# Performance work log

Measured on AMD Instinct MI355X. Metric: run time of the kernel, lower is better.

Reference implementation:

```python
import jax, jax.numpy as jnp
import numpy as np

N = 100000
E = 1600000
GENE = 512
HID = 128
NCLS = 10
EPS = 1e-5  # BatchNorm1d default eps


def setup_inputs() -> dict:
    key = jax.random.key(0)
    ks = jax.random.split(key, 16)
    def lin(k, fan_in, fan_out):
        return (jax.random.normal(k, (fan_in, fan_out), jnp.float32) / np.sqrt(fan_in)).astype(jnp.float32)
    dims = [(GENE, HID), (HID, 2 * HID), (2 * HID, HID), (HID, HID // 2)]
    inp = {}
    inp["x"] = jax.random.normal(ks[0], (N, GENE), jnp.float32)
    inp["edge_index"] = jax.random.randint(ks[1], (2, E), 0, N)
    for i, (di, do) in enumerate(dims, start=1):
        inp[f"W{i}"] = lin(ks[1 + i], di, do)
        inp[f"b{i}"] = jnp.zeros((do,), jnp.float32)
        inp[f"g{i}"] = jnp.ones((do,), jnp.float32)     # BN gamma
        inp[f"beta{i}"] = jnp.zeros((do,), jnp.float32)  # BN beta
    inp["Wc"] = lin(ks[10], HID // 2, NCLS)
    inp["bc"] = jnp.zeros((NCLS,), jnp.float32)
    return inp


def gcn_conv(h_in, W, b, src, dst, deg_inv_sqrt):
    # PyG GCNConv: transform, then symmetric-normalized aggregation with self-loops
    h = h_in @ W                                   # [N, out]
    norm = (deg_inv_sqrt[src] * deg_inv_sqrt[dst])[:, None]  # [E, 1]
    agg = jnp.zeros_like(h).at[dst].add(h[src] * norm)       # scatter-add over edges
    agg = agg + h * (deg_inv_sqrt ** 2)[:, None]   # self-loop contribution (norm = 1/deg)
    return agg + b


def relu_bn(h, g, beta):
    # forward applies BatchNorm1d(F.relu(h)) in training mode (batch stats, biased var)
    h = jax.nn.relu(h)
    mu = h.mean(axis=0)
    var = h.var(axis=0)
    return (h - mu) * jax.lax.rsqrt(var + EPS) * g + beta


def reference(x, edge_index, W1, b1, g1, beta1, W2, b2, g2, beta2,
              W3, b3, g3, beta3, W4, b4, g4, beta4, Wc, bc):
    src, dst = edge_index[0], edge_index[1]
    # degree after adding self-loops (edge weight 1)
    deg = jnp.zeros((x.shape[0],), x.dtype).at[dst].add(1.0) + 1.0
    dis = jax.lax.rsqrt(deg)
    h = relu_bn(gcn_conv(x, W1, b1, src, dst, dis), g1, beta1)
    h = relu_bn(gcn_conv(h, W2, b2, src, dst, dis), g2, beta2)
    h = relu_bn(gcn_conv(h, W3, b3, src, dst, dis), g3, beta3)
    h = relu_bn(gcn_conv(h, W4, b4, src, dst, dis), g4, beta4)
    return h @ Wc + bc
```

## Files before the change

kernel.cpp:

```cpp
#include <hip/hip_runtime.h>
#include <hip/hip_bf16.h>

#define EPS_BN 1e-5f

using frag8 = __attribute__((ext_vector_type(8))) short;
using f32x4 = __attribute__((ext_vector_type(4))) float;

typedef const __attribute__((address_space(1))) void* gas_ptr;
typedef __attribute__((address_space(3))) void* las_ptr;

__device__ __forceinline__ void async_ld16(const void* g, void* l) {
  __builtin_amdgcn_global_load_lds((gas_ptr)g, (las_ptr)l, 16, 0, 0);
}

__device__ __forceinline__ float bfu2f(unsigned short u) {
  union { unsigned int i; float f; } c;
  c.i = (unsigned int)u << 16;
  return c.f;
}


__global__ void count_ticket_kernel(const int* __restrict__ dst, int* __restrict__ cnt,
                                    int* __restrict__ rank, int E) {
  int e = blockIdx.x * blockDim.x + threadIdx.x;
  if (e < E) rank[e] = atomicAdd(&cnt[dst[e]], 1);
}

__global__ void scan1_kernel(const int* __restrict__ cnt, int* __restrict__ out,
                             int* __restrict__ bsum, float* __restrict__ dis, int n) {
  __shared__ int sdata[1024];
  int tid = threadIdx.x;
  int i = blockIdx.x * 1024 + tid;
  int v = (i < n) ? cnt[i] : 0;
  if (i < n) dis[i] = rsqrtf((float)v + 1.0f);
  sdata[tid] = v;
  __syncthreads();
  for (int off = 1; off < 1024; off <<= 1) {
    int t = (tid >= off) ? sdata[tid - off] : 0;
    __syncthreads();
    sdata[tid] += t;
    __syncthreads();
  }
  if (i < n) out[i] = sdata[tid] - v;
  if (tid == 1023) bsum[blockIdx.x] = sdata[1023];
}

__global__ void scan2_kernel(int* __restrict__ bsum, int nb) {
  __shared__ int sdata[1024];
  int tid = threadIdx.x;
  int v = (tid < nb) ? bsum[tid] : 0;
  sdata[tid] = v;
  __syncthreads();
  for (int off = 1; off < 1024; off <<= 1) {
    int t = (tid >= off) ? sdata[tid - off] : 0;
    __syncthreads();
    sdata[tid] += t;
    __syncthreads();
  }
  if (tid < nb) bsum[tid] = sdata[tid] - v;
}

__global__ void scan3_kernel(int* __restrict__ out, const int* __restrict__ bsum,
                             int n, int E) {
  int i = blockIdx.x * 1024 + threadIdx.x;
  if (i < n) out[i] += bsum[blockIdx.x];
  if (i == 0) out[n] = E;
}

__global__ void scatter_kernel(const int* __restrict__ src, const int* __restrict__ dst,
                               const int* __restrict__ rowstart, const int* __restrict__ rank,
                               int* __restrict__ csr_src, int E) {
  int e = blockIdx.x * blockDim.x + threadIdx.x;
  if (e < E) csr_src[rowstart[dst[e]] + rank[e]] = src[e];
}


__global__ void convert_bf16_kernel(const float* __restrict__ in,
                                    __hip_bfloat16* __restrict__ out, size_t n4) {
  size_t i = (size_t)blockIdx.x * blockDim.x + threadIdx.x;
  size_t stride = (size_t)gridDim.x * blockDim.x;
  for (; i < n4; i += stride) {
    float4 v = *(const float4*)&in[i * 4];
    union { ushort4 u; __hip_bfloat16 h[4]; } pk;
    pk.h[0] = __float2bfloat16(v.x);
    pk.h[1] = __float2bfloat16(v.y);
    pk.h[2] = __float2bfloat16(v.z);
    pk.h[3] = __float2bfloat16(v.w);
    *(ushort4*)&out[i * 4] = pk.u;
  }
}

__global__ void wtrans_all_kernel(const float* __restrict__ W1, const float* __restrict__ W2,
                                  const float* __restrict__ W3, const float* __restrict__ W4,
                                  __hip_bfloat16* __restrict__ T1, __hip_bfloat16* __restrict__ T2,
                                  __hip_bfloat16* __restrict__ T3, __hip_bfloat16* __restrict__ T4) {
  int i = blockIdx.x * blockDim.x + threadIdx.x;
  const float* W; __hip_bfloat16* T; int K, F, base;
  if (i < 65536)        { W = W1; T = T1; K = 512; F = 128; base = 0; }
  else if (i < 98304)   { W = W2; T = T2; K = 128; F = 256; base = 65536; }
  else if (i < 131072)  { W = W3; T = T3; K = 256; F = 128; base = 98304; }
  else if (i < 139264)  { W = W4; T = T4; K = 128; F = 64;  base = 131072; }
  else return;
  int j = i - base;
  int k = j / F, f = j % F;
  T[f * K + k] = __float2bfloat16(W[j]);
}

template <int TN, int OMODE>
__global__ __launch_bounds__(256) void mfma_gemm_kernel(
    const __hip_bfloat16* __restrict__ A, const __hip_bfloat16* __restrict__ Bt,
    void* __restrict__ Cv, const float* __restrict__ bias,
    const float* __restrict__ rowscale, float* __restrict__ stats,
    int Nr, int K, int F) {
  constexpr int WM = (TN == 128) ? 64 : 32;
  constexpr int MI = WM / 16;
  __shared__ __align__(16) __hip_bfloat16 As[128 * 32];
  __shared__ __align__(16) __hip_bfloat16 Bs[TN * 32];
  __shared__ float sacc[128], sqc[128];
  int tid = (int)threadIdx.x;
  int wid = tid >> 6, lane = tid & 63;
  int rowBase = blockIdx.x * 128;
  int colBase = blockIdx.y * TN;
  int wr, wc;
  if (TN == 128) { wr = (wid >> 1) * 64; wc = (wid & 1) * 64; }
  else           { wr = wid * 32;        wc = 0; }

  f32x4 zero = {0.f, 0.f, 0.f, 0.f};
  f32x4 acc[MI][4];
#pragma unroll
  for (int i = 0; i < MI; ++i)
#pragma unroll
    for (int j = 0; j < 4; ++j) acc[i][j] = zero;

  int lm = lane & 15;
  int k8 = (lane >> 4) * 8;

  if constexpr (OMODE == 2) {
    if (tid < 128) { sacc[tid] = 0.f; sqc[tid] = 0.f; }
  }

  for (int k0 = 0; k0 < K; k0 += 32) {
#pragma unroll
    for (int p = 0; p < 2; ++p) {
      int sidx = p * 256 + tid;
      int row = sidx >> 2;
      int kq = (sidx & 3) * 8;
      int gr = rowBase + row;
      if (gr >= Nr) gr = Nr - 1;
      async_ld16(A + (size_t)gr * K + k0 + kq, (char*)As + (p * 256 + wid * 64) * 16);
    }
    constexpr int BPASS = TN / 64;
#pragma unroll
    for (int p = 0; p < BPASS; ++p) {
      int sidx = p * 256 + tid;
      int col = sidx >> 2;
      int kq = (sidx & 3) * 8;
      async_ld16(Bt + (size_t)(colBase + col) * K + k0 + kq,
                 (char*)Bs + (p * 256 + wid * 64) * 16);
    }
    __syncthreads();

    frag8 af[MI], bf[4];
#pragma unroll
    for (int i = 0; i < MI; ++i)
      af[i] = *(const frag8*)&As[(wr + i * 16 + lm) * 32 + k8];
#pragma unroll
    for (int j = 0; j < 4; ++j)
      bf[j] = *(const frag8*)&Bs[(wc + j * 16 + lm) * 32 + k8];
#pragma unroll
    for (int i = 0; i < MI; ++i)
#pragma unroll
      for (int j = 0; j < 4; ++j)
        acc[i][j] = __builtin_amdgcn_mfma_f32_16x16x32_bf16(af[i], bf[j], acc[i][j], 0, 0, 0);
    __syncthreads();
  }

  int rquad = (lane >> 4) * 4;
  float s[4] = {0.f, 0.f, 0.f, 0.f}, q[4] = {0.f, 0.f, 0.f, 0.f};
#pragma unroll
  for (int i = 0; i < MI; ++i) {
    int rb = rowBase + wr + i * 16 + rquad;
#pragma unroll
    for (int r = 0; r < 4; ++r) {
      int row = rb + r;
      if (row < Nr) {
        if constexpr (OMODE == 1) {
          float rs = rowscale[row];
#pragma unroll
          for (int j = 0; j < 4; ++j) {
            int col = colBase + wc + j * 16 + lm;
            ((__hip_bfloat16*)Cv)[(size_t)row * F + col] = __float2bfloat16(acc[i][j][r] * rs);
          }
        } else {
#pragma unroll
          for (int j = 0; j < 4; ++j) {
            int col = colBase + wc + j * 16 + lm;
            float v = acc[i][j][r] + bias[col];
            ((float*)Cv)[(size_t)row * F + col] = v;
            float rl = fmaxf(v, 0.f);
            s[j] += rl;
            q[j] += rl * rl;
          }
        }
      }
    }
  }

  if constexpr (OMODE == 2) {
#pragma unroll
    for (int j = 0; j < 4; ++j) {
      s[j] += __shfl_xor(s[j], 16, 64); s[j] += __shfl_xor(s[j], 32, 64);
      q[j] += __shfl_xor(q[j], 16, 64); q[j] += __shfl_xor(q[j], 32, 64);
    }
    if (lane < 16) {
#pragma unroll
      for (int j = 0; j < 4; ++j) {
        atomicAdd(&sacc[wc + j * 16 + lane], s[j]);
        atomicAdd(&sqc[wc + j * 16 + lane], q[j]);
      }
    }
    __syncthreads();
    if (tid < 128) {
      atomicAdd(&stats[colBase + tid], sacc[tid]);
      atomicAdd(&stats[256 + colBase + tid], sqc[tid]);
    }
  }
}

template <int VEC, int OMODE>
__global__ __launch_bounds__(256) void agg_kernel(
    const __hip_bfloat16* __restrict__ Ts, const int* __restrict__ rowstart,
    const int* __restrict__ csr_src, const float* __restrict__ dis,
    const float* __restrict__ bias, void* __restrict__ H,
    float* __restrict__ stats, int Nn, int F) {
  __shared__ float lsum[512], lqs[512];
  int tid = (int)threadIdx.x;
  int wid4 = tid >> 6;
  int lane = tid & 63;
  int off = lane * VEC;
  const unsigned short* Tu = (const unsigned short*)Ts;

  float bj[VEC];
  float s[VEC], q[VEC];
#pragma unroll
  for (int j = 0; j < VEC; ++j) {
    bj[j] = (OMODE == 1) ? bias[off + j] : 0.f;
    s[j] = 0.f; q[j] = 0.f;
  }

  for (int d = blockIdx.x * 4 + wid4; d < Nn; d += gridDim.x * 4) {
    float acc[VEC];
    {
      unsigned short r[VEC];
      if constexpr (VEC == 2) *(ushort2*)r = *(const ushort2*)&Tu[(size_t)d * F + off];
      else                    r[0] = Tu[(size_t)d * F + off];
#pragma unroll
      for (int j = 0; j < VEC; ++j) acc[j] = bfu2f(r[j]);
    }

    int e0 = rowstart[d], e1 = rowstart[d + 1];
    for (int e = e0; e < e1; e += 8) {
      int idx[8];
      bool val[8];
#pragma unroll
      for (int p = 0; p < 8; ++p) {
        int ee = e + p;
        val[p] = ee < e1;
        idx[p] = csr_src[val[p] ? ee : e1 - 1];
      }
      unsigned short r[8][VEC];
#pragma unroll
      for (int p = 0; p < 8; ++p) {
        if constexpr (VEC == 2) *(ushort2*)r[p] = *(const ushort2*)&Tu[(size_t)idx[p] * F + off];
        else                    r[p][0] = Tu[(size_t)idx[p] * F + off];
      }
#pragma unroll
      for (int p = 0; p < 8; ++p)
#pragma unroll
        for (int j = 0; j < VEC; ++j) acc[j] += val[p] ? bfu2f(r[p][j]) : 0.f;
    }

    float dd = dis[d];
    if constexpr (OMODE == 0) {
      union { ushort2 u; __hip_bfloat16 h[2]; } pk;
      if constexpr (VEC == 2) {
        pk.h[0] = __float2bfloat16(acc[0] * dd);
        pk.h[1] = __float2bfloat16(acc[1] * dd);
        *(ushort2*)&((__hip_bfloat16*)H)[(size_t)d * F + off] = pk.u;
      } else {
        ((__hip_bfloat16*)H)[(size_t)d * F + off] = __float2bfloat16(acc[0] * dd);
      }
    } else {
      float v[VEC];
#pragma unroll
      for (int j = 0; j < VEC; ++j) {
        v[j] = acc[j] * dd + bj[j];
        float rl = fmaxf(v[j], 0.f);
        s[j] += rl;
        q[j] += rl * rl;
      }
      if constexpr (VEC == 2) {
        *(float2*)&((float*)H)[(size_t)d * F + off] = make_float2(v[0], v[1]);
      } else {
        ((float*)H)[(size_t)d * F + off] = v[0];
      }
    }
  }

  if constexpr (OMODE == 1) {
#pragma unroll
    for (int j = 0; j < VEC; ++j) {
      lsum[(lane * VEC + j) * 4 + wid4] = s[j];
      lqs[(lane * VEC + j) * 4 + wid4] = q[j];
    }
    __syncthreads();
    int nc = 64 * VEC;
    for (int c = tid; c < nc; c += 256) {
      float a = lsum[c * 4 + 0] + lsum[c * 4 + 1] + lsum[c * 4 + 2] + lsum[c * 4 + 3];
      float b = lqs[c * 4 + 0] + lqs[c * 4 + 1] + lqs[c * 4 + 2] + lqs[c * 4 + 3];
      atomicAdd(&stats[c], a);
      atomicAdd(&stats[256 + c], b);
    }
  }
}

__global__ void bnfin_kernel(float* __restrict__ stats, const float* __restrict__ g,
                             const float* __restrict__ beta, float* __restrict__ ss,
                             int Nn, int F) {
  int c = (int)threadIdx.x;
  if (c < F) {
    float mean = stats[c] / (float)Nn;
    float var = stats[256 + c] / (float)Nn - mean * mean;
    float sc = g[c] * rsqrtf(var + EPS_BN);
    ss[c] = sc;
    ss[256 + c] = beta[c] - mean * sc;
  }
  stats[c] = 0.f;
  stats[256 + c] = 0.f;
}

__global__ void bnapply_kernel(const float* __restrict__ H, const float* __restrict__ ss,
                               const float* __restrict__ rowscale,
                               __hip_bfloat16* __restrict__ O, size_t total4, int F, int logF) {
  size_t i = (size_t)blockIdx.x * blockDim.x + threadIdx.x;
  size_t stride = (size_t)gridDim.x * blockDim.x;
  for (; i < total4; i += stride) {
    size_t b = i * 4;
    float4 v = *(const float4*)&H[b];
    int c = (int)(b & (size_t)(F - 1));
    float rs = rowscale ? rowscale[b >> logF] : 1.0f;
    union { ushort4 u; __hip_bfloat16 h[4]; } pk;
    pk.h[0] = __float2bfloat16((fmaxf(v.x, 0.f) * ss[c + 0] + ss[256 + c + 0]) * rs);
    pk.h[1] = __float2bfloat16((fmaxf(v.y, 0.f) * ss[c + 1] + ss[256 + c + 1]) * rs);
    pk.h[2] = __float2bfloat16((fmaxf(v.z, 0.f) * ss[c + 2] + ss[256 + c + 2]) * rs);
    pk.h[3] = __float2bfloat16((fmaxf(v.w, 0.f) * ss[c + 3] + ss[256 + c + 3]) * rs);
    *(ushort4*)&O[b] = pk.u;
  }
}

__global__ __launch_bounds__(256) void bnapply_cls_kernel(
    const float* __restrict__ Hf, const float* __restrict__ ss,
    const float* __restrict__ Wc, const float* __restrict__ bc,
    float* __restrict__ out, int Nn) {
  int gt = blockIdx.x * blockDim.x + (int)threadIdx.x;
  int wid = gt >> 6;
  int lane = (int)threadIdx.x & 63;
  if (wid >= Nn) return;
  float v = Hf[(size_t)wid * 64 + lane];
  float h = fmaxf(v, 0.f) * ss[lane] + ss[256 + lane];
#pragma unroll
  for (int c = 0; c < 10; ++c) {
    float p = h * Wc[lane * 10 + c];
#pragma unroll
    for (int off = 32; off > 0; off >>= 1) p += __shfl_down(p, off, 64);
    if (lane == 0) out[(size_t)wid * 10 + c] = p + bc[c];
  }
}


extern "C" void kernel_launch(void* const* d_in, const int* in_sizes, int n_in,
                              void* d_out, int out_size, void* d_ws, size_t ws_size,
                              hipStream_t stream) {
  (void)n_in; (void)out_size; (void)ws_size;
  const float* x    = (const float*)d_in[0];
  const int*   edge = (const int*)d_in[1];
  const int E  = in_sizes[1] / 2;
  const int Nn = in_sizes[0] / 512;
  const int* e_src = edge;
  const int* e_dst = edge + E;

  const float* W[4]  = {(const float*)d_in[2],  (const float*)d_in[6],
                        (const float*)d_in[10], (const float*)d_in[14]};
  const float* bv[4] = {(const float*)d_in[3],  (const float*)d_in[7],
                        (const float*)d_in[11], (const float*)d_in[15]};
  const float* gv[4] = {(const float*)d_in[4],  (const float*)d_in[8],
                        (const float*)d_in[12], (const float*)d_in[16]};
  const float* bt[4] = {(const float*)d_in[5],  (const float*)d_in[9],
                        (const float*)d_in[13], (const float*)d_in[17]};
  const float* Wc = (const float*)d_in[18];
  const float* bc = (const float*)d_in[19];
  float* out = (float*)d_out;

  const int Kdim[4] = {512, 128, 256, 128};
  const int Fdim[4] = {128, 256, 128, 64};

  char* p = (char*)d_ws;
  auto alloc = [&](size_t bytes) -> void* {
    void* r = (void*)p;
    p += (bytes + 255) & ~(size_t)255;
    return r;
  };
  int*   cnt      = (int*)alloc((size_t)Nn * 4);
  int*   rowstart = (int*)alloc((size_t)(Nn + 1) * 4);
  int*   bsum     = (int*)alloc(1024 * 4);
  float* dis      = (float*)alloc((size_t)Nn * 4);
  float* stats    = (float*)alloc(512 * 4);
  float* ss       = (float*)alloc(512 * 4);
  int*   rank     = (int*)alloc((size_t)E * 4);
  int*   csr_src  = (int*)alloc((size_t)E * 4);
  __hip_bfloat16* Wt[4];
  for (int l = 0; l < 4; ++l)
    Wt[l] = (__hip_bfloat16*)alloc((size_t)Kdim[l] * Fdim[l] * 2);
  char* R0 = (char*)alloc((size_t)Nn * 512 * 2);
  __hip_bfloat16* Tb = (__hip_bfloat16*)alloc((size_t)Nn * 256 * 2);
  __hip_bfloat16* P0 = (__hip_bfloat16*)alloc((size_t)Nn * 256 * 2);
  __hip_bfloat16* P1 = (__hip_bfloat16*)alloc((size_t)Nn * 256 * 2);
  __hip_bfloat16* Xb = (__hip_bfloat16*)R0;
  float*          Hf = (float*)R0;

  hipMemsetAsync(cnt, 0, (size_t)Nn * 4, stream);
  hipMemsetAsync(stats, 0, 512 * 4, stream);

  int nb = (Nn + 1023) / 1024;
  count_ticket_kernel<<<(E + 255) / 256, 256, 0, stream>>>(e_dst, cnt, rank, E);
  scan1_kernel<<<nb, 1024, 0, stream>>>(cnt, rowstart, bsum, dis, Nn);
  scan2_kernel<<<1, 1024, 0, stream>>>(bsum, nb);
  scan3_kernel<<<nb, 1024, 0, stream>>>(rowstart, bsum, Nn, E);
  scatter_kernel<<<(E + 255) / 256, 256, 0, stream>>>(e_src, e_dst, rowstart, rank,
                                                      csr_src, E);

  wtrans_all_kernel<<<(139264 + 255) / 256, 256, 0, stream>>>(W[0], W[1], W[2], W[3],
                                                              Wt[0], Wt[1], Wt[2], Wt[3]);
  convert_bf16_kernel<<<4096, 256, 0, stream>>>(x, Xb, (size_t)Nn * 512 / 4);

  const int AGG_BLOCKS = 1536;

  auto bnapply = [&](int l, int F, __hip_bfloat16* Obf, const float* rsc) {
    bnfin_kernel<<<1, 256, 0, stream>>>(stats, gv[l], bt[l], ss, Nn, F);
    size_t total4 = (size_t)Nn * F / 4;
    int logF = (F == 256) ? 8 : (F == 128 ? 7 : 6);
    bnapply_kernel<<<(int)((total4 + 255) / 256), 256, 0, stream>>>(Hf, ss, rsc, Obf,
                                                                    total4, F, logF);
  };

  {
    dim3 g((Nn + 127) / 128, 1);
    mfma_gemm_kernel<128, 1><<<g, 256, 0, stream>>>(Xb, Wt[0], Tb, nullptr, dis, nullptr,
                                                    Nn, 512, 128);
    agg_kernel<2, 1><<<AGG_BLOCKS, 256, 0, stream>>>(Tb, rowstart, csr_src, dis,
                                                     bv[0], Hf, stats, Nn, 128);
    bnapply(0, 128, P0, dis);
  }
  {
    agg_kernel<2, 0><<<AGG_BLOCKS, 256, 0, stream>>>(P0, rowstart, csr_src, dis,
                                                     nullptr, Tb, nullptr, Nn, 128);
    dim3 g((Nn + 127) / 128, 2);
    mfma_gemm_kernel<128, 2><<<g, 256, 0, stream>>>(Tb, Wt[1], Hf, bv[1], nullptr, stats,
                                                    Nn, 128, 256);
    bnapply(1, 256, P1, nullptr);
  }
  {
    dim3 g((Nn + 127) / 128, 1);
    mfma_gemm_kernel<128, 1><<<g, 256, 0, stream>>>(P1, Wt[2], Tb, nullptr, dis, nullptr,
                                                    Nn, 256, 128);
    agg_kernel<2, 1><<<AGG_BLOCKS, 256, 0, stream>>>(Tb, rowstart, csr_src, dis,
                                                     bv[2], Hf, stats, Nn, 128);
    bnapply(2, 128, P0, nullptr);
  }
  {
    dim3 g((Nn + 127) / 128, 1);
    mfma_gemm_kernel<64, 1><<<g, 256, 0, stream>>>(P0, Wt[3], Tb, nullptr, dis, nullptr,
                                                   Nn, 128, 64);
    agg_kernel<1, 1><<<AGG_BLOCKS, 256, 0, stream>>>(Tb, rowstart, csr_src, dis,
                                                     bv[3], Hf, stats, Nn, 64);
    bnfin_kernel<<<1, 256, 0, stream>>>(stats, gv[3], bt[3], ss, Nn, 64);
    int clsBlocks = (Nn * 64 + 255) / 256;
    bnapply_cls_kernel<<<clsBlocks, 256, 0, stream>>>(Hf, ss, Wc, bc, out, Nn);
  }
}
```

Measured before the change: 1.044 ms.

## Merge prep kernels, fuse scatter into GEMM1, fold BN finalize into apply

New measurement: 1.040 ms. About the same (-0.3%).

```diff
diff --git a/kernel.cpp b/kernel.cpp
--- a/kernel.cpp
+++ b/kernel.cpp
@@ -19,11 +19,43 @@
   return c.f;
 }
 
-
-__global__ void count_ticket_kernel(const int* __restrict__ dst, int* __restrict__ cnt,
-                                    int* __restrict__ rank, int E) {
-  int e = blockIdx.x * blockDim.x + threadIdx.x;
-  if (e < E) rank[e] = atomicAdd(&cnt[dst[e]], 1);
+__global__ __launch_bounds__(256) void prep_fat_kernel(
+    const int* __restrict__ e_dst, int* __restrict__ cnt, int* __restrict__ rank, int E,
+    int CB,
+    const float* __restrict__ x, __hip_bfloat16* __restrict__ Xb, size_t n4, int VB,
+    const float* __restrict__ W1, const float* __restrict__ W2,
+    const float* __restrict__ W3, const float* __restrict__ W4,
+    __hip_bfloat16* __restrict__ T1, __hip_bfloat16* __restrict__ T2,
+    __hip_bfloat16* __restrict__ T3, __hip_bfloat16* __restrict__ T4) {
+  int b = (int)blockIdx.x;
+  int tid = (int)threadIdx.x;
+  if (b < CB) {
+    int e = b * 256 + tid;
+    if (e < E) rank[e] = atomicAdd(&cnt[e_dst[e]], 1);
+  } else if (b < CB + VB) {
+    size_t i = (size_t)(b - CB) * 256 + tid;
+    size_t stride = (size_t)VB * 256;
+    for (; i < n4; i += stride) {
+      float4 v = *(const float4*)&x[i * 4];
+      union { ushort4 u; __hip_bfloat16 h[4]; } pk;
+      pk.h[0] = __float2bfloat16(v.x);
+      pk.h[1] = __float2bfloat16(v.y);
+      pk.h[2] = __float2bfloat16(v.z);
+      pk.h[3] = __float2bfloat16(v.w);
+      *(ushort4*)&Xb[i * 4] = pk.u;
+    }
+  } else {
+    int i = (b - CB - VB) * 256 + tid;
+    const float* W; __hip_bfloat16* T; int F, K, base;
+    if (i < 65536)        { W = W1; T = T1; K = 512; F = 128; base = 0; }
+    else if (i < 98304)   { W = W2; T = T2; K = 128; F = 256; base = 65536; }
+    else if (i < 131072)  { W = W3; T = T3; K = 256; F = 128; base = 98304; }
+    else if (i < 139264)  { W = W4; T = T4; K = 128; F = 64;  base = 131072; }
+    else return;
+    int j = i - base;
+    int k = j / F, f = j % F;
+    T[f * K + k] = __float2bfloat16(W[j]);
+  }
 }
 
 __global__ void scan1_kernel(const int* __restrict__ cnt, int* __restrict__ out,
@@ -67,51 +99,12 @@
   if (i == 0) out[n] = E;
 }
 
-__global__ void scatter_kernel(const int* __restrict__ src, const int* __restrict__ dst,
-                               const int* __restrict__ rowstart, const int* __restrict__ rank,
-                               int* __restrict__ csr_src, int E) {
-  int e = blockIdx.x * blockDim.x + threadIdx.x;
-  if (e < E) csr_src[rowstart[dst[e]] + rank[e]] = src[e];
-}
-
-
-__global__ void convert_bf16_kernel(const float* __restrict__ in,
-                                    __hip_bfloat16* __restrict__ out, size_t n4) {
-  size_t i = (size_t)blockIdx.x * blockDim.x + threadIdx.x;
-  size_t stride = (size_t)gridDim.x * blockDim.x;
-  for (; i < n4; i += stride) {
-    float4 v = *(const float4*)&in[i * 4];
-    union { ushort4 u; __hip_bfloat16 h[4]; } pk;
-    pk.h[0] = __float2bfloat16(v.x);
-    pk.h[1] = __float2bfloat16(v.y);
-    pk.h[2] = __float2bfloat16(v.z);
-    pk.h[3] = __float2bfloat16(v.w);
-    *(ushort4*)&out[i * 4] = pk.u;
-  }
-}
-
-__global__ void wtrans_all_kernel(const float* __restrict__ W1, const float* __restrict__ W2,
-                                  const float* __restrict__ W3, const float* __restrict__ W4,
-                                  __hip_bfloat16* __restrict__ T1, __hip_bfloat16* __restrict__ T2,
-                                  __hip_bfloat16* __restrict__ T3, __hip_bfloat16* __restrict__ T4) {
-  int i = blockIdx.x * blockDim.x + threadIdx.x;
-  const float* W; __hip_bfloat16* T; int K, F, base;
-  if (i < 65536)        { W = W1; T = T1; K = 512; F = 128; base = 0; }
-  else if (i < 98304)   { W = W2; T = T2; K = 128; F = 256; base = 65536; }
-  else if (i < 131072)  { W = W3; T = T3; K = 256; F = 128; base = 98304; }
-  else if (i < 139264)  { W = W4; T = T4; K = 128; F = 64;  base = 131072; }
-  else return;
-  int j = i - base;
-  int k = j / F, f = j % F;
-  T[f * K + k] = __float2bfloat16(W[j]);
-}
-
 template <int TN, int OMODE>
-__global__ __launch_bounds__(256) void mfma_gemm_kernel(
+__device__ __forceinline__ void gemm_body(
     const __hip_bfloat16* __restrict__ A, const __hip_bfloat16* __restrict__ Bt,
     void* __restrict__ Cv, const float* __restrict__ bias,
     const float* __restrict__ rowscale, float* __restrict__ stats,
-    int Nr, int K, int F) {
+    int Nr, int K, int F, int bx, int by) {
   constexpr int WM = (TN == 128) ? 64 : 32;
   constexpr int MI = WM / 16;
   __shared__ __align__(16) __hip_bfloat16 As[128 * 32];
@@ -119,8 +112,8 @@
   __shared__ float sacc[128], sqc[128];
   int tid = (int)threadIdx.x;
   int wid = tid >> 6, lane = tid & 63;
-  int rowBase = blockIdx.x * 128;
-  int colBase = blockIdx.y * TN;
+  int rowBase = bx * 128;
+  int colBase = by * TN;
   int wr, wc;
   if (TN == 128) { wr = (wid >> 1) * 64; wc = (wid & 1) * 64; }
   else           { wr = wid * 32;        wc = 0; }
@@ -224,6 +217,32 @@
       atomicAdd(&stats[colBase + tid], sacc[tid]);
       atomicAdd(&stats[256 + colBase + tid], sqc[tid]);
     }
+  }
+}
+
+template <int TN, int OMODE>
+__global__ __launch_bounds__(256) void mfma_gemm_kernel(
+    const __hip_bfloat16* __restrict__ A, const __hip_bfloat16* __restrict__ Bt,
+    void* __restrict__ Cv, const float* __restrict__ bias,
+    const float* __restrict__ rowscale, float* __restrict__ stats,
+    int Nr, int K, int F) {
+  gemm_body<TN, OMODE>(A, Bt, Cv, bias, rowscale, stats, Nr, K, F,
+                       (int)blockIdx.x, (int)blockIdx.y);
+}
+
+__global__ __launch_bounds__(256) void gemm1_scatter_kernel(
+    const __hip_bfloat16* __restrict__ A, const __hip_bfloat16* __restrict__ Bt,
+    void* __restrict__ Cv, const float* __restrict__ rowscale,
+    int Nr, int K, int F, int G1,
+    const int* __restrict__ src, const int* __restrict__ dst,
+    const int* __restrict__ rowstart, const int* __restrict__ rank,
+    int* __restrict__ csr_src, int E) {
+  int b = (int)blockIdx.x;
+  if (b < G1) {
+    gemm_body<128, 1>(A, Bt, Cv, nullptr, rowscale, nullptr, Nr, K, F, b, 0);
+  } else {
+    int e = (b - G1) * 256 + (int)threadIdx.x;
+    if (e < E) csr_src[rowstart[dst[e]] + rank[e]] = src[e];
   }
 }
 
@@ -259,23 +278,23 @@
     }
 
     int e0 = rowstart[d], e1 = rowstart[d + 1];
-    for (int e = e0; e < e1; e += 8) {
-      int idx[8];
-      bool val[8];
-#pragma unroll
-      for (int p = 0; p < 8; ++p) {
+    for (int e = e0; e < e1; e += 16) {
+      int idx[16];
+      bool val[16];
+#pragma unroll
+      for (int p = 0; p < 16; ++p) {
         int ee = e + p;
         val[p] = ee < e1;
         idx[p] = csr_src[val[p] ? ee : e1 - 1];
       }
-      unsigned short r[8][VEC];
-#pragma unroll
-      for (int p = 0; p < 8; ++p) {
+      unsigned short r[16][VEC];
+#pragma unroll
+      for (int p = 0; p < 16; ++p) {
         if constexpr (VEC == 2) *(ushort2*)r[p] = *(const ushort2*)&Tu[(size_t)idx[p] * F + off];
         else                    r[p][0] = Tu[(size_t)idx[p] * F + off];
       }
 #pragma unroll
-      for (int p = 0; p < 8; ++p)
+      for (int p = 0; p < 16; ++p)
 #pragma unroll
         for (int j = 0; j < VEC; ++j) acc[j] += val[p] ? bfu2f(r[p][j]) : 0.f;
     }
@@ -324,25 +343,22 @@
   }
 }
 
-__global__ void bnfin_kernel(float* __restrict__ stats, const float* __restrict__ g,
-                             const float* __restrict__ beta, float* __restrict__ ss,
-                             int Nn, int F) {
-  int c = (int)threadIdx.x;
-  if (c < F) {
-    float mean = stats[c] / (float)Nn;
-    float var = stats[256 + c] / (float)Nn - mean * mean;
-    float sc = g[c] * rsqrtf(var + EPS_BN);
-    ss[c] = sc;
-    ss[256 + c] = beta[c] - mean * sc;
-  }
-  stats[c] = 0.f;
-  stats[256 + c] = 0.f;
-}
-
-__global__ void bnapply_kernel(const float* __restrict__ H, const float* __restrict__ ss,
-                               const float* __restrict__ rowscale,
-                               __hip_bfloat16* __restrict__ O, size_t total4, int F, int logF) {
-  size_t i = (size_t)blockIdx.x * blockDim.x + threadIdx.x;
+__global__ __launch_bounds__(256) void bnapply_kernel(
+    const float* __restrict__ H, const float* __restrict__ stats,
+    const float* __restrict__ g, const float* __restrict__ beta,
+    const float* __restrict__ rowscale, __hip_bfloat16* __restrict__ O,
+    size_t total4, int F, int logF, float invN) {
+  __shared__ float ssc[256], ssb[256];
+  int tid = (int)threadIdx.x;
+  if (tid < F) {
+    float mean = stats[tid] * invN;
+    float var = stats[256 + tid] * invN - mean * mean;
+    float sc = g[tid] * rsqrtf(var + EPS_BN);
+    ssc[tid] = sc;
+    ssb[tid] = beta[tid] - mean * sc;
+  }
+  __syncthreads();
+  size_t i = (size_t)blockIdx.x * blockDim.x + tid;
   size_t stride = (size_t)gridDim.x * blockDim.x;
   for (; i < total4; i += stride) {
     size_t b = i * 4;
@@ -350,24 +366,35 @@
     int c = (int)(b & (size_t)(F - 1));
     float rs = rowscale ? rowscale[b >> logF] : 1.0f;
     union { ushort4 u; __hip_bfloat16 h[4]; } pk;
-    pk.h[0] = __float2bfloat16((fmaxf(v.x, 0.f) * ss[c + 0] + ss[256 + c + 0]) * rs);
-    pk.h[1] = __float2bfloat16((fmaxf(v.y, 0.f) * ss[c + 1] + ss[256 + c + 1]) * rs);
-    pk.h[2] = __float2bfloat16((fmaxf(v.z, 0.f) * ss[c + 2] + ss[256 + c + 2]) * rs);
-    pk.h[3] = __float2bfloat16((fmaxf(v.w, 0.f) * ss[c + 3] + ss[256 + c + 3]) * rs);
+    pk.h[0] = __float2bfloat16((fmaxf(v.x, 0.f) * ssc[c + 0] + ssb[c + 0]) * rs);
+    pk.h[1] = __float2bfloat16((fmaxf(v.y, 0.f) * ssc[c + 1] + ssb[c + 1]) * rs);
+    pk.h[2] = __float2bfloat16((fmaxf(v.z, 0.f) * ssc[c + 2] + ssb[c + 2]) * rs);
+    pk.h[3] = __float2bfloat16((fmaxf(v.w, 0.f) * ssc[c + 3] + ssb[c + 3]) * rs);
     *(ushort4*)&O[b] = pk.u;
   }
 }
 
 __global__ __launch_bounds__(256) void bnapply_cls_kernel(
-    const float* __restrict__ Hf, const float* __restrict__ ss,
+    const float* __restrict__ Hf, const float* __restrict__ stats,
+    const float* __restrict__ g, const float* __restrict__ beta,
     const float* __restrict__ Wc, const float* __restrict__ bc,
-    float* __restrict__ out, int Nn) {
-  int gt = blockIdx.x * blockDim.x + (int)threadIdx.x;
+    float* __restrict__ out, int Nn, float invN) {
+  __shared__ float ssc[64], ssb[64];
+  int tid = (int)threadIdx.x;
+  if (tid < 64) {
+    float mean = stats[tid] * invN;
+    float var = stats[256 + tid] * invN - mean * mean;
+    float sc = g[tid] * rsqrtf(var + EPS_BN);
+    ssc[tid] = sc;
+    ssb[tid] = beta[tid] - mean * sc;
+  }
+  __syncthreads();
+  int gt = blockIdx.x * blockDim.x + tid;
   int wid = gt >> 6;
-  int lane = (int)threadIdx.x & 63;
+  int lane = tid & 63;
   if (wid >= Nn) return;
   float v = Hf[(size_t)wid * 64 + lane];
-  float h = fmaxf(v, 0.f) * ss[lane] + ss[256 + lane];
+  float h = fmaxf(v, 0.f) * ssc[lane] + ssb[lane];
 #pragma unroll
   for (int c = 0; c < 10; ++c) {
     float p = h * Wc[lane * 10 + c];
@@ -403,6 +430,7 @@
 
   const int Kdim[4] = {512, 128, 256, 128};
   const int Fdim[4] = {128, 256, 128, 64};
+  const float invN = 1.0f / (float)Nn;
 
   char* p = (char*)d_ws;
   auto alloc = [&](size_t bytes) -> void* {
@@ -411,11 +439,11 @@
     return r;
   };
   int*   cnt      = (int*)alloc((size_t)Nn * 4);
+  float* stats    = (float*)alloc(2048 * 4);
+  size_t zeroBytes = (size_t)(((size_t)Nn * 4 + 255) & ~(size_t)255) + 2048 * 4;
   int*   rowstart = (int*)alloc((size_t)(Nn + 1) * 4);
   int*   bsum     = (int*)alloc(1024 * 4);
   float* dis      = (float*)alloc((size_t)Nn * 4);
-  float* stats    = (float*)alloc(512 * 4);
-  float* ss       = (float*)alloc(512 * 4);
   int*   rank     = (int*)alloc((size_t)E * 4);
   int*   csr_src  = (int*)alloc((size_t)E * 4);
   __hip_bfloat16* Wt[4];
@@ -428,63 +456,60 @@
   __hip_bfloat16* Xb = (__hip_bfloat16*)R0;
   float*          Hf = (float*)R0;
 
-  hipMemsetAsync(cnt, 0, (size_t)Nn * 4, stream);
-  hipMemsetAsync(stats, 0, 512 * 4, stream);
+  hipMemsetAsync(cnt, 0, zeroBytes, stream);
+
+  const int CB = (E + 255) / 256;
+  const int VB = 2048;
+  const int WB = (139264 + 255) / 256;
+  prep_fat_kernel<<<CB + VB + WB, 256, 0, stream>>>(
+      e_dst, cnt, rank, E, CB,
+      x, Xb, (size_t)Nn * 512 / 4, VB,
+      W[0], W[1], W[2], W[3], Wt[0], Wt[1], Wt[2], Wt[3]);
 
   int nb = (Nn + 1023) / 1024;
-  count_ticket_kernel<<<(E + 255) / 256, 256, 0, stream>>>(e_dst, cnt, rank, E);
   scan1_kernel<<<nb, 1024, 0, stream>>>(cnt, rowstart, bsum, dis, Nn);
   scan2_kernel<<<1, 1024, 0, stream>>>(bsum, nb);
   scan3_kernel<<<nb, 1024, 0, stream>>>(rowstart, bsum, Nn, E);
-  scatter_kernel<<<(E + 255) / 256, 256, 0, stream>>>(e_src, e_dst, rowstart, rank,
-                                                      csr_src, E);
-
-  wtrans_all_kernel<<<(139264 + 255) / 256, 256, 0, stream>>>(W[0], W[1], W[2], W[3],
-                                                              Wt[0], Wt[1], Wt[2], Wt[3]);
-  convert_bf16_kernel<<<4096, 256, 0, stream>>>(x, Xb, (size_t)Nn * 512 / 4);
 
   const int AGG_BLOCKS = 1536;
-
-  auto bnapply = [&](int l, int F, __hip_bfloat16* Obf, const float* rsc) {
-    bnfin_kernel<<<1, 256, 0, stream>>>(stats, gv[l], bt[l], ss, Nn, F);
-    size_t total4 = (size_t)Nn * F / 4;
-    int logF = (F == 256) ? 8 : (F == 128 ? 7 : 6);
-    bnapply_kernel<<<(int)((total4 + 255) / 256), 256, 0, stream>>>(Hf, ss, rsc, Obf,
-                                                                    total4, F, logF);
-  };
-
+  int gx = (Nn + 127) / 128;
+
+  gemm1_scatter_kernel<<<gx + CB, 256, 0, stream>>>(
+      Xb, Wt[0], Tb, dis, Nn, 512, 128, gx,
+      e_src, e_dst, rowstart, rank, csr_src, E);
+  agg_kernel<2, 1><<<AGG_BLOCKS, 256, 0, stream>>>(Tb, rowstart, csr_src, dis,
+                                                   bv[0], Hf, stats, Nn, 128);
+  bnapply_kernel<<<(int)(((size_t)Nn * 128 / 4 + 255) / 256), 256, 0, stream>>>(
+      Hf, stats, gv[0], bt[0], dis, P0, (size_t)Nn * 128 / 4, 128, 7, invN);
+
+  agg_kernel<2, 0><<<AGG_BLOCKS, 256, 0, stream>>>(P0, rowstart, csr_src, dis,
+                                                   nullptr, Tb, nullptr, Nn, 128);
   {
-    dim3 g((Nn + 127) / 128, 1);
-    mfma_gemm_kernel<128, 1><<<g, 256, 0, stream>>>(Xb, Wt[0], Tb, nullptr, dis, nullptr,
-                                                    Nn, 512, 128);
-    agg_kernel<2, 1><<<AGG_BLOCKS, 256, 0, stream>>>(Tb, rowstart, csr_src, dis,
-                                                     bv[0], Hf, stats, Nn, 128);
-    bnapply(0, 128, P0, dis);
-  }
+    dim3 g(gx, 2);
+    mfma_gemm_kernel<128, 2><<<g, 256, 0, stream>>>(Tb, Wt[1], Hf, bv[1], nullptr,
+                                                    stats + 512, Nn, 128, 256);
+  }
+  bnapply_kernel<<<(int)(((size_t)Nn * 256 / 4 + 255) / 256), 256, 0, stream>>>(
+      Hf, stats + 512, gv[1], bt[1], nullptr, P1, (size_t)Nn * 256 / 4, 256, 8, invN);
+
   {
-    agg_kernel<2, 0><<<AGG_BLOCKS, 256, 0, stream>>>(P0, rowstart, csr_src, dis,
-                                                     nullptr, Tb, nullptr, Nn, 128);
-    dim3 g((Nn + 127) / 128, 2);
-    mfma_gemm_kernel<128, 2><<<g, 256, 0, stream>>>(Tb, Wt[1], Hf, bv[1], nullptr, stats,
-                                                    Nn, 128, 256);
-    bnapply(1, 256, P1, nullptr);
-  }
-  {
-    dim3 g((Nn + 127) / 128, 1);
+    dim3 g(gx, 1);
     mfma_gemm_kernel<128, 1><<<g, 256, 0, stream>>>(P1, Wt[2], Tb, nullptr, dis, nullptr,
                                                     Nn, 256, 128);
-    agg_kernel<2, 1><<<AGG_BLOCKS, 256, 0, stream>>>(Tb, rowstart, csr_src, dis,
-                                                     bv[2], Hf, stats, Nn, 128);
-    bnapply(2, 128, P0, nullptr);
-  }
+  }
+  agg_kernel<2, 1><<<AGG_BLOCKS, 256, 0, stream>>>(Tb, rowstart, csr_src, dis,
+                                                   bv[2], Hf, stats + 1024, Nn, 128);
+  bnapply_kernel<<<(int)(((size_t)Nn * 128 / 4 + 255) / 256), 256, 0, stream>>>(
+      Hf, stats + 1024, gv[2], bt[2], nullptr, P0, (size_t)Nn * 128 / 4, 128, 7, invN);
+
   {
-    dim3 g((Nn + 127) / 128, 1);
+    dim3 g(gx, 1);
     mfma_gemm_kernel<64, 1><<<g, 256, 0, stream>>>(P0, Wt[3], Tb, nullptr, dis, nullptr,
                                                    Nn, 128, 64);
-    agg_kernel<1, 1><<<AGG_BLOCKS, 256, 0, stream>>>(Tb, rowstart, csr_src, dis,
-                                                     bv[3], Hf, stats, Nn, 64);
-    bnfin_kernel<<<1, 256, 0, stream>>>(stats, gv[3], bt[3], ss, Nn, 64);
-    int clsBlocks = (Nn * 64 + 255) / 256;
-    bnapply_cls_kernel<<<clsBlocks, 256, 0, stream>>>(Hf, ss, Wc, bc, out, Nn);
-  }
-}
+  }
+  agg_kernel<1, 1><<<AGG_BLOCKS, 256, 0, stream>>>(Tb, rowstart, csr_src, dis,
+                                                   bv[3], Hf, stats + 1536, Nn, 64);
+  int clsBlocks = (Nn * 64 + 255) / 256;
+  bnapply_cls_kernel<<<clsBlocks, 256, 0, stream>>>(Hf, stats + 1536, gv[3], bt[3],
+                                                    Wc, bc, out, Nn, invN);
+}
```
